# Performance work log

Hardware: AMD Instinct MI355X
Metric: run time of the kernel (lower is better)

Reference implementation:

```python
import jax, jax.numpy as jnp
import numpy as np

# Mistral-7B layer-0 config
D, DKV, DFF, NH, NKV, HD, BLK, VOCAB = 4096, 1024, 14336, 32, 8, 128, 64, 32000
THETA = 10000.0
NF4_CODE = jnp.array([-1.0, -0.6961928009986877, -0.5250730514526367, -0.39491748809814453,
                      -0.28444138169288635, -0.18477343022823334, -0.09105003625154495, 0.0,
                      0.07958029955625534, 0.16093020141124725, 0.24611230194568634,
                      0.33791524171829224, 0.44070982933044434, 0.5626170039176941,
                      0.7229568362236023, 1.0], dtype=jnp.float32)


def dequant_nf4(idx, absmax):
    # idx: int [out,in] 4-bit codes; absmax: [numel/BLK] blockwise scales
    w = jnp.take(NF4_CODE, idx.reshape(-1, BLK)) * absmax[:, None]
    return w.reshape(idx.shape)


def rmsnorm(x, w, eps=1e-5):
    return x * jax.lax.rsqrt(jnp.mean(x * x, axis=-1, keepdims=True) + eps) * w


def rope(x, pos):
    # x: [B,S,H,HD] -- HF rotate-half convention
    half = HD // 2
    inv = 1.0 / (THETA ** (jnp.arange(0, half, dtype=jnp.float32) / half))
    f = pos[:, None] * inv[None, :]                      # [S, half]
    cos = jnp.concatenate([jnp.cos(f), jnp.cos(f)], -1)[None, :, None, :]
    sin = jnp.concatenate([jnp.sin(f), jnp.sin(f)], -1)[None, :, None, :]
    x1, x2 = x[..., :half], x[..., half:]
    rot = jnp.concatenate([-x2, x1], -1)
    return x * cos + rot * sin


def setup_inputs() -> dict:
    key = jax.random.key(0)
    ks = jax.random.split(key, 20)
    B, S = 4, 512
    inp = {}
    inp["input_ids"] = jax.random.randint(ks[0], (B, S), 0, VOCAB, dtype=jnp.int32)
    inp["attention_mask"] = jnp.ones((B, S), dtype=jnp.int32)
    inp["embed_table"] = jax.random.normal(ks[1], (VOCAB, D), dtype=jnp.float32) * 0.02
    shapes = {"q": (D, D), "k": (DKV, D), "v": (DKV, D), "o": (D, D),
              "gate": (DFF, D), "up": (DFF, D), "down": (D, DFF)}
    for i, (n, sh) in enumerate(shapes.items()):
        inp["idx_" + n] = jax.random.randint(ks[2 + i], sh, 0, 16, dtype=jnp.int32)
        inp["absmax_" + n] = jax.random.uniform(ks[9 + i], (sh[0] * sh[1] // BLK,), dtype=jnp.float32) * 0.02
    inp["rms1_w"] = jnp.ones((D,), jnp.float32)
    inp["rms2_w"] = jnp.ones((D,), jnp.float32)
    inp["dp_w"] = jax.random.normal(ks[16], (50, D), jnp.float32) * 0.02
    inp["dp_b"] = jnp.zeros((50,), jnp.float32)
    return inp


def reference(input_ids, attention_mask, embed_table,
              idx_q, idx_k, idx_v, idx_o, idx_gate, idx_up, idx_down,
              absmax_q, absmax_k, absmax_v, absmax_o, absmax_gate, absmax_up, absmax_down,
              rms1_w, rms2_w, dp_w, dp_b):
    B, S = input_ids.shape
    h = embed_table[input_ids]                            # [B,S,D]

    # --- Mistral decoder layer 0 (hidden_states[1]) ---
    r = rmsnorm(h, rms1_w)
    Wq = dequant_nf4(idx_q, absmax_q)
    Wk = dequant_nf4(idx_k, absmax_k)
    Wv = dequant_nf4(idx_v, absmax_v)
    Wo = dequant_nf4(idx_o, absmax_o)
    q = (r @ Wq.T).reshape(B, S, NH, HD)
    k = (r @ Wk.T).reshape(B, S, NKV, HD)
    v = (r @ Wv.T).reshape(B, S, NKV, HD)
    pos = jnp.arange(S, dtype=jnp.float32)
    q, k = rope(q, pos), rope(k, pos)
    rep = NH // NKV
    k = jnp.repeat(k, rep, axis=2)
    v = jnp.repeat(v, rep, axis=2)
    scores = jnp.einsum('bqhd,bkhd->bhqk', q, k) / np.float32(np.sqrt(HD))
    causal = jnp.tril(jnp.ones((S, S), bool))
    m = causal[None, None] & (attention_mask[:, None, None, :] > 0)
    scores = jnp.where(m, scores, jnp.float32(-1e9))
    p = jax.nn.softmax(scores, axis=-1)
    ao = jnp.einsum('bhqk,bkhd->bqhd', p, v).reshape(B, S, D)
    h = h + ao @ Wo.T

    r2 = rmsnorm(h, rms2_w)
    Wg = dequant_nf4(idx_gate, absmax_gate)
    Wu = dequant_nf4(idx_up, absmax_up)
    Wd = dequant_nf4(idx_down, absmax_down)
    h = h + (jax.nn.silu(r2 @ Wg.T) * (r2 @ Wu.T)) @ Wd.T

    # --- last_token_pool + L2 normalize ---
    last = jnp.sum(attention_mask, axis=-1) - 1           # [B]
    pooled = h[jnp.arange(B), last]                       # [B,D]
    pooled = pooled / jnp.maximum(jnp.linalg.norm(pooled, axis=1, keepdims=True), 1e-12)

    # --- down_projection + query*entity node embeddings ---
    emb = pooled @ dp_w.T + dp_b                          # [B,50]
    bs = B // 2
    node = emb[:bs] * emb[bs:]                            # [bs,50]
    return node
```

## Files before the change

### kernel.cpp

```cpp
#include <hip/hip_runtime.h>
#include <stdint.h>
#include <math.h>

#define TOK 2048
#define DMODEL 4096
#define DFF 14336
#define SEQ 512

typedef float f32x4 __attribute__((ext_vector_type(4)));
typedef float f32x2 __attribute__((ext_vector_type(2)));
typedef short s16x8 __attribute__((ext_vector_type(8)));
typedef unsigned short u16x8 __attribute__((ext_vector_type(8)));

__constant__ float NF4_TAB[16] = {
  -1.0f, -0.6961928009986877f, -0.5250730514526367f, -0.39491748809814453f,
  -0.28444138169288635f, -0.18477343022823334f, -0.09105003625154495f, 0.0f,
  0.07958029955625534f, 0.16093020141124725f, 0.24611230194568634f,
  0.33791524171829224f, 0.44070982933044434f, 0.5626170039176941f,
  0.7229568362236023f, 1.0f };

__device__ __forceinline__ uint16_t f2bf(float f) {
  union { float f; uint32_t u; } x; x.f = f;
  uint32_t r = (x.u + 0x7FFFu + ((x.u >> 16) & 1u)) >> 16;
  return (uint16_t)r;
}
__device__ __forceinline__ float bf2f(uint16_t u) {
  union { uint32_t u; float f; } x; x.u = ((uint32_t)u) << 16;
  return x.f;
}
__device__ __forceinline__ f32x4 mfma16(s16x8 a, s16x8 b, f32x4 c) {
  return __builtin_amdgcn_mfma_f32_16x16x32_bf16(a, b, c, 0, 0, 0);
}
__device__ __forceinline__ void gload_lds16(const void* g, void* l) {
  __builtin_amdgcn_global_load_lds(
    (const __attribute__((address_space(1))) unsigned int*)g,
    (__attribute__((address_space(3))) unsigned int*)l, 16, 0, 0);
}
__device__ __forceinline__ f32x2 pf(float w, f32x2 v, f32x2 acc) {
  f32x2 wv = {w, w};
  return wv * v + acc;
}

__global__ __launch_bounds__(256) void k_fusedA(const int* __restrict__ ids,
    const float* __restrict__ table, const float* __restrict__ w1,
    uint16_t* __restrict__ rbuf, const int* __restrict__ idxK,
    const float* __restrict__ amK, const int* __restrict__ idxV,
    const float* __restrict__ amV, uint16_t* __restrict__ wbuf,
    const int* __restrict__ maskp, int* __restrict__ lastb)
{
  int bid = blockIdx.x, tid = threadIdx.x;
  if (bid < 2048) {
    int t = bid;
    int wv = tid >> 6, l = tid & 63;
    const float* src = table + (size_t)ids[t] * DMODEL;
    int d0 = tid * 16;
    float vals[16];
    float ss = 0.f;
    #pragma unroll
    for (int i = 0; i < 4; ++i) {
      float4 v4 = *(const float4*)(src + d0 + i * 4);
      vals[i*4+0] = v4.x; vals[i*4+1] = v4.y; vals[i*4+2] = v4.z; vals[i*4+3] = v4.w;
      ss += v4.x*v4.x + v4.y*v4.y + v4.z*v4.z + v4.w*v4.w;
    }
    #pragma unroll
    for (int off = 1; off < 64; off <<= 1) ss += __shfl_xor(ss, off);
    __shared__ float red[4];
    if (l == 0) red[wv] = ss;
    __syncthreads();
    float rs = rsqrtf((red[0]+red[1]+red[2]+red[3]) * (1.f/DMODEL) + 1e-5f);
    #pragma unroll
    for (int cth = 0; cth < 2; ++cth) {
      int dd = d0 + cth * 8;
      u16x8 pk;
      #pragma unroll
      for (int j = 0; j < 8; ++j) pk[j] = f2bf(vals[cth*8+j] * rs * w1[dd + j]);
      int dsw = (dd & ~63) | (((((dd >> 3) & 7) ^ (t & 7))) << 3);
      *(u16x8*)(rbuf + (size_t)t * DMODEL + dsw) = pk;
    }
  } else if (bid < 3072) {
    bool isV = bid >= 2560;
    const int* idx = isV ? idxV : idxK;
    const float* am = isV ? amV : amK;
    uint16_t* out = wbuf + (isV ? (size_t)1024 * DMODEL : 0);
    int base = bid - (isV ? 2560 : 2048);
    __shared__ float code[16];
    if (tid < 16) code[tid] = NF4_TAB[tid];
    __syncthreads();
    const int nch = 1024 * DMODEL / 8;
    for (int c = base * 256 + tid; c < nch; c += 512 * 256) {
      int e = c << 3;
      int row = e >> 12;
      int kc = e & 4095;
      float a = am[c >> 3];
      int4 i0 = *(const int4*)(idx + e);
      int4 i1 = *(const int4*)(idx + e + 4);
      u16x8 pk;
      pk[0] = f2bf(code[i0.x] * a);
      pk[1] = f2bf(code[i0.y] * a);
      pk[2] = f2bf(code[i0.z] * a);
      pk[3] = f2bf(code[i0.w] * a);
      pk[4] = f2bf(code[i1.x] * a);
      pk[5] = f2bf(code[i1.y] * a);
      pk[6] = f2bf(code[i1.z] * a);
      pk[7] = f2bf(code[i1.w] * a);
      int dk = (kc & ~63) | (((((kc >> 3) & 7) ^ (row & 7))) << 3);
      *(u16x8*)(out + (size_t)row * DMODEL + dk) = pk;
    }
  } else {
    int b = bid - 3072;
    if (tid < 64) {
      int cnt = 0;
      for (int j = tid; j < SEQ; j += 64) cnt += (maskp[b * SEQ + j] > 0);
      #pragma unroll
      for (int off = 1; off < 64; off <<= 1) cnt += __shfl_xor(cnt, off);
      if (tid == 0) lastb[b] = cnt - 1;
    }
  }
}

__global__ __launch_bounds__(512, 2) void k_gemmkv(
    const uint16_t* __restrict__ A, const uint16_t* __restrict__ W,
    float* __restrict__ pout)
{
  constexpr int K = 4096;
  constexpr int NT = 16;
  __shared__ __align__(1024) uint16_t As_[2 * 256 * 64];
  __shared__ __align__(1024) uint16_t Bs_[2 * 256 * 64];
  const int tid = threadIdx.x;
  const int wid = tid >> 6, l = tid & 63;
  const int wr = wid >> 2, wc = wid & 3;
  int f = blockIdx.x + (blockIdx.y << 3) + (blockIdx.z << 6);
  int fs = ((f & 7) << 5) + (f >> 3);
  const int n0 = (fs & 7) * 256;
  const int m0 = ((fs >> 3) & 7) * 256;
  const int zq = fs >> 6;
  const size_t kbase = (size_t)zq * 1024;
  const int lrow = l >> 3, lcb = (l & 7) * 16;

  auto stA = [&](int t, int h) {
    int ta = (t < NT) ? t : (t - NT);
    const char* g = (const char*)A +
        ((size_t)(m0 + h * 128 + wid * 16 + lrow) * K + kbase + ta * 64) * 2 + lcb;
    char* s = (char*)As_ + (t & 1) * 32768 + h * 16384 + wid * 2048;
    gload_lds16(g, s);
    gload_lds16(g + (size_t)8 * K * 2, s + 1024);
  };
  auto stB = [&](int t, int h) {
    int ta = (t < NT) ? t : (t - NT);
    const char* g = (const char*)W +
        ((size_t)(n0 + h * 128 + wid * 16 + lrow) * K + kbase + ta * 64) * 2 + lcb;
    char* s = (char*)Bs_ + (t & 1) * 32768 + h * 16384 + wid * 2048;
    gload_lds16(g, s);
    gload_lds16(g + (size_t)8 * K * 2, s + 1024);
  };

  const int cb0 = (((l >> 4) << 4)) ^ ((l & 7) << 4);
  const int cb1 = (64 + ((l >> 4) << 4)) ^ ((l & 7) << 4);

  const f32x4 Z4 = {0.f, 0.f, 0.f, 0.f};
// ... 36 lines not shown
  }

  stB(0, 0); stA(0, 0); stB(0, 1); stA(0, 1);
  stB(1, 0); stA(1, 0); stB(1, 1);
  VMW;
  __builtin_amdgcn_s_barrier();

  for (int it = 0; it < NT / 2; ++it) {
    int t0 = 2 * it, t1 = t0 + 1;
    PHASE(0, 0, 1, stA(t1, 1));
    PHASE(0, 1, 0, stB(t0 + 2, 0));
    PHASE(0, 2, 0, stA(t0 + 2, 0));
    PHASE(0, 3, 0, { stB(t0 + 2, 1); VMW; });
    PHASE(1, 0, 1, stA(t0 + 2, 1));
    PHASE(1, 1, 0, stB(t1 + 2, 0));
    PHASE(1, 2, 0, stA(t1 + 2, 0));
    PHASE(1, 3, 0, { stB(t1 + 2, 1); VMW; });
  }
  asm volatile("s_waitcnt vmcnt(0)" ::: "memory");
  __builtin_amdgcn_s_barrier();
#undef PHASE
#undef VMW

  float* po = pout + (size_t)zq * 2048 * 2048;
  #pragma unroll
  for (int mf = 0; mf < 8; ++mf)
    #pragma unroll
    for (int nf = 0; nf < 4; ++nf)
      #pragma unroll
      for (int r = 0; r < 4; ++r) {
        int row = m0 + (2 * mf + wr) * 16 + ((l >> 4) << 2) + r;
        int col = n0 + wc * 64 + nf * 16 + (l & 15);
        po[(size_t)row * 2048 + col] = acc[mf][nf][r];
      }
}

__global__ __launch_bounds__(256) void k_prep_r4(const uint16_t* __restrict__ rbuf,
    const int* __restrict__ lastb, float* __restrict__ r4i)
{
  int r = blockIdx.x;
  int t = r * SEQ + lastb[r];
  const uint16_t* src = rbuf + (size_t)t * DMODEL;
  for (int k = threadIdx.x * 8; k < DMODEL; k += 2048) {
    int so = (k & ~63) | (((((k >> 3) & 7) ^ (t & 7))) << 3);
    u16x8 v = *(const u16x8*)(src + so);
    #pragma unroll
    for (int j = 0; j < 8; ++j) r4i[(k + j) * 4 + r] = bf2f(v[j]);
  }
}

__global__ __launch_bounds__(256) void k_fusedD(const float* __restrict__ p,
    uint16_t* __restrict__ kv, const int* __restrict__ idxQ,
    const float* __restrict__ amQ, const float* __restrict__ a4i,
    float* __restrict__ q4i)
{
  int bid = blockIdx.x, tid = threadIdx.x;
  if (bid < 2048) {
    int t = bid;
    const size_t zs = (size_t)2048 * 2048;
    auto sum4 = [&](int c) -> float {
      size_t o = (size_t)t * 2048 + c;
      return p[o] + p[o + zs] + p[o + 2 * zs] + p[o + 3 * zs];
    };
    float pos = (float)(t & (SEQ - 1));
    for (int pi = tid; pi < 512; pi += 256) {
      int hh = pi >> 6, j = pi & 63;
      int c1 = hh * 128 + j, c2 = c1 + 64;
      float s1 = sum4(c1), s2 = sum4(c2);
      float f = pos * expf(-(float)j * 0.14391156831212787f);
      float sn, cs;
      sincosf(f, &sn, &cs);
      kv[(size_t)t * 2048 + c1] = f2bf(s1 * cs - s2 * sn);
      kv[(size_t)t * 2048 + c2] = f2bf(s2 * cs + s1 * sn);
    }
    for (int c = 1024 + tid; c < 2048; c += 256)
      kv[(size_t)t * 2048 + c] = f2bf(sum4(c));
  } else {
    __shared__ float code[16];
    if (tid < 16) code[tid] = NF4_TAB[tid];
    __syncthreads();
    int wv = tid >> 6, l = tid & 63;
    int lhi = l >> 4;
    int n = (bid - 2048) * 4 + wv;
    const int4* ip = (const int4*)(idxQ + (size_t)n * 4096);
    const float* ap = amQ + (size_t)n * 64;
    f32x2 a01 = {0.f, 0.f}, a23 = {0.f, 0.f};
    #pragma unroll
    for (int kk = 0; kk < 16; ++kk) {
      int4 iv = ip[kk * 64 + l];
      float sc = ap[kk * 4 + lhi];
      float w0 = code[iv.x] * sc, w1 = code[iv.y] * sc;
      float w2 = code[iv.z] * sc, w3 = code[iv.w] * sc;
      const float* A0 = a4i + (kk * 256 + l * 4) * 4;
      f32x4 k0 = *(const f32x4*)(A0);
      f32x4 k1 = *(const f32x4*)(A0 + 4);
      f32x4 k2 = *(const f32x4*)(A0 + 8);
      f32x4 k3 = *(const f32x4*)(A0 + 12);
      a01 = pf(w0, __builtin_shufflevector(k0, k0, 0, 1), a01);
      a23 = pf(w0, __builtin_shufflevector(k0, k0, 2, 3), a23);
      a01 = pf(w1, __builtin_shufflevector(k1, k1, 0, 1), a01);
      a23 = pf(w1, __builtin_shufflevector(k1, k1, 2, 3), a23);
      a01 = pf(w2, __builtin_shufflevector(k2, k2, 0, 1), a01);
      a23 = pf(w2, __builtin_shufflevector(k2, k2, 2, 3), a23);
      a01 = pf(w3, __builtin_shufflevector(k3, k3, 0, 1), a01);
      a23 = pf(w3, __builtin_shufflevector(k3, k3, 2, 3), a23);
    }
    float a0 = a01[0], a1 = a01[1], a2 = a23[0], a3 = a23[1];
    #pragma unroll
    for (int off = 1; off < 64; off <<= 1) {
      a0 += __shfl_xor(a0, off); a1 += __shfl_xor(a1, off);
      a2 += __shfl_xor(a2, off); a3 += __shfl_xor(a3, off);
    }
    if (l == 0) {
      f32x4 o;
      o[0] = a0; o[1] = a1; o[2] = a2; o[3] = a3;
      *(f32x4*)(q4i + (size_t)n * 4) = o;
    }
  }
}

__global__ __launch_bounds__(256) void k_gemv_o(const int* __restrict__ idx,
    const float* __restrict__ am, const float* __restrict__ a4i,
    float* __restrict__ out4i, const float* __restrict__ table,
    const int* __restrict__ ids, const int* __restrict__ lastb)
{
  __shared__ float code[16];
  if (threadIdx.x < 16) code[threadIdx.x] = NF4_TAB[threadIdx.x];
  __syncthreads();
  int wv = threadIdx.x >> 6, l = threadIdx.x & 63;
  int lhi = l >> 4;
  int n = blockIdx.x * 4 + wv;
  const int4* ip = (const int4*)(idx + (size_t)n * 4096);
  const float* ap = am + (size_t)n * 64;
  f32x2 a01 = {0.f, 0.f}, a23 = {0.f, 0.f};
  #pragma unroll
  for (int kk = 0; kk < 16; ++kk) {
    int4 iv = ip[kk * 64 + l];
    float sc = ap[kk * 4 + lhi];
    float w0 = code[iv.x] * sc, w1 = code[iv.y] * sc;
    float w2 = code[iv.z] * sc, w3 = code[iv.w] * sc;
// ... 9 lines not shown
    a01 = pf(w2, __builtin_shufflevector(k2, k2, 0, 1), a01);
    a23 = pf(w2, __builtin_shufflevector(k2, k2, 2, 3), a23);
    a01 = pf(w3, __builtin_shufflevector(k3, k3, 0, 1), a01);
    a23 = pf(w3, __builtin_shufflevector(k3, k3, 2, 3), a23);
  }
  float a0 = a01[0], a1 = a01[1], a2 = a23[0], a3 = a23[1];
  #pragma unroll
  for (int off = 1; off < 64; off <<= 1) {
    a0 += __shfl_xor(a0, off); a1 += __shfl_xor(a1, off);
    a2 += __shfl_xor(a2, off); a3 += __shfl_xor(a3, off);
  }
  if (l == 0) {
    f32x4 o;
    o[0] = a0; o[1] = a1; o[2] = a2; o[3] = a3;
    #pragma unroll
    for (int r = 0; r < 4; ++r)
      o[r] += table[(size_t)ids[r * SEQ + lastb[r]] * DMODEL + n];
    *(f32x4*)(out4i + (size_t)n * 4) = o;
  }
}

__global__ __launch_bounds__(256) void k_gemv_gu(const int* __restrict__ idxg,
    const float* __restrict__ amg, const int* __restrict__ idxu,
    const float* __restrict__ amu, const float* __restrict__ a4i,
    float* __restrict__ hm4i)
{
  __shared__ float code[16];
  if (threadIdx.x < 16) code[threadIdx.x] = NF4_TAB[threadIdx.x];
  __syncthreads();
  int wv = threadIdx.x >> 6, l = threadIdx.x & 63;
  int lhi = l >> 4;
  int n = blockIdx.x * 4 + wv;
  const int4* ipg = (const int4*)(idxg + (size_t)n * 4096);
  const int4* ipu = (const int4*)(idxu + (size_t)n * 4096);
  const float* apg = amg + (size_t)n * 64;
  const float* apu = amu + (size_t)n * 64;
  f32x2 g01 = {0.f, 0.f}, g23 = {0.f, 0.f};
  f32x2 u01 = {0.f, 0.f}, u23 = {0.f, 0.f};
  #pragma unroll 8
  for (int kk = 0; kk < 16; ++kk) {
    int4 ig = ipg[kk * 64 + l];
    int4 iu = ipu[kk * 64 + l];
    float sg = apg[kk * 4 + lhi];
    float su = apu[kk * 4 + lhi];
    float wg0 = code[ig.x] * sg, wg1 = code[ig.y] * sg;
    float wg2 = code[ig.z] * sg, wg3 = code[ig.w] * sg;
    float wu0 = code[iu.x] * su, wu1 = code[iu.y] * su;
    float wu2 = code[iu.z] * su, wu3 = code[iu.w] * su;
    const float* A0 = a4i + (kk * 256 + l * 4) * 4;
    f32x4 k0 = *(const f32x4*)(A0);
    f32x4 k1 = *(const f32x4*)(A0 + 4);
    f32x4 k2 = *(const f32x4*)(A0 + 8);
    f32x4 k3 = *(const f32x4*)(A0 + 12);
    f32x2 k0l = __builtin_shufflevector(k0, k0, 0, 1), k0h = __builtin_shufflevector(k0, k0, 2, 3);
    f32x2 k1l = __builtin_shufflevector(k1, k1, 0, 1), k1h = __builtin_shufflevector(k1, k1, 2, 3);
    f32x2 k2l = __builtin_shufflevector(k2, k2, 0, 1), k2h = __builtin_shufflevector(k2, k2, 2, 3);
    f32x2 k3l = __builtin_shufflevector(k3, k3, 0, 1), k3h = __builtin_shufflevector(k3, k3, 2, 3);
    g01 = pf(wg0, k0l, g01); g23 = pf(wg0, k0h, g23);
    g01 = pf(wg1, k1l, g01); g23 = pf(wg1, k1h, g23);
    g01 = pf(wg2, k2l, g01); g23 = pf(wg2, k2h, g23);
    g01 = pf(wg3, k3l, g01); g23 = pf(wg3, k3h, g23);
    u01 = pf(wu0, k0l, u01); u23 = pf(wu0, k0h, u23);
    u01 = pf(wu1, k1l, u01); u23 = pf(wu1, k1h, u23);
    u01 = pf(wu2, k2l, u01); u23 = pf(wu2, k2h, u23);
    u01 = pf(wu3, k3l, u01); u23 = pf(wu3, k3h, u23);
  }
  float g0 = g01[0], g1 = g01[1], g2 = g23[0], g3 = g23[1];
  float u0 = u01[0], u1 = u01[1], u2 = u23[0], u3 = u23[1];
  #pragma unroll
  for (int off = 1; off < 64; off <<= 1) {
    g0 += __shfl_xor(g0, off); g1 += __shfl_xor(g1, off);
    g2 += __shfl_xor(g2, off); g3 += __shfl_xor(g3, off);
    u0 += __shfl_xor(u0, off); u1 += __shfl_xor(u1, off);
    u2 += __shfl_xor(u2, off); u3 += __shfl_xor(u3, off);
  }
  if (l == 0) {
// ... 34 lines not shown
    a23 = pf(w0, __builtin_shufflevector(k0, k0, 2, 3), a23);
    a01 = pf(w1, __builtin_shufflevector(k1, k1, 0, 1), a01);
    a23 = pf(w1, __builtin_shufflevector(k1, k1, 2, 3), a23);
    a01 = pf(w2, __builtin_shufflevector(k2, k2, 0, 1), a01);
    a23 = pf(w2, __builtin_shufflevector(k2, k2, 2, 3), a23);
    a01 = pf(w3, __builtin_shufflevector(k3, k3, 0, 1), a01);
    a23 = pf(w3, __builtin_shufflevector(k3, k3, 2, 3), a23);
  }
  float a0 = a01[0], a1 = a01[1], a2 = a23[0], a3 = a23[1];
  #pragma unroll
  for (int off = 1; off < 64; off <<= 1) {
    a0 += __shfl_xor(a0, off); a1 += __shfl_xor(a1, off);
    a2 += __shfl_xor(a2, off); a3 += __shfl_xor(a3, off);
  }
  if (l == 0) {
    f32x4 hr = *(const f32x4*)(h4i + (size_t)n * 4);
    h4r[0 * 4096 + n] = hr[0] + a0;
    h4r[1 * 4096 + n] = hr[1] + a1;
    h4r[2 * 4096 + n] = hr[2] + a2;
    h4r[3 * 4096 + n] = hr[3] + a3;
  }
}

__global__ __launch_bounds__(256) void k_attn4(const float* __restrict__ q4i,
    const uint16_t* __restrict__ kv, const int* __restrict__ maskp,
    const int* __restrict__ lastb, float* __restrict__ ao4i)
{
  int hh = blockIdx.x, b = blockIdx.y;
  int kvh = hh >> 2;
  int tid = threadIdx.x;
  __shared__ float qs[128];
  __shared__ float sarr[512];
  __shared__ float red[256];
  __shared__ f32x2 oacc2[4][64];
  int last = lastb[b];
  if (tid < 128) {
    int d = tid, j = d & 63;
    float f = (float)last * expf(-(float)j * 0.14391156831212787f);
    float sn, cs;
    sincosf(f, &sn, &cs);
    float qd  = q4i[(hh * 128 + d) * 4 + b];
    float qd2 = (d < 64) ? q4i[(hh * 128 + d + 64) * 4 + b]
                         : q4i[(hh * 128 + d - 64) * 4 + b];
    float v = (d < 64) ? (qd * cs - qd2 * sn) : (qd * cs + qd2 * sn);
    qs[d] = v * 0.08838834764831845f;
  }
  __syncthreads();
  float sl[2];
  #pragma unroll
  for (int h2 = 0; h2 < 2; ++h2) {
    int jj = tid + h2 * 256;
    bool valid = (jj <= last) && (maskp[b * SEQ + jj] > 0);
    float s = -1e9f;
    if (valid) {
      s = 0.f;
      const uint16_t* kp = kv + ((size_t)(b * SEQ + jj)) * 2048 + kvh * 128;
      #pragma unroll
      for (int c = 0; c < 16; ++c) {
        u16x8 kvv = *(const u16x8*)(kp + c * 8);
        #pragma unroll
        for (int e = 0; e < 8; ++e)
          s = fmaf(qs[c * 8 + e], bf2f(kvv[e]), s);
      }
    }
    sarr[jj] = s;
    sl[h2] = s;
  }
  red[tid] = fmaxf(sl[0], sl[1]);
  __syncthreads();
  for (int s = 128; s > 0; s >>= 1) {
    if (tid < s) red[tid] = fmaxf(red[tid], red[tid + s]);
    __syncthreads();
  }
  float m = red[0];
  __syncthreads();
  float ps = 0.f;
  #pragma unroll
  for (int h2 = 0; h2 < 2; ++h2) {
    int jj = tid + h2 * 256;
    float pe = __expf(sarr[jj] - m);
    ps += pe;
    sarr[jj] = pe;
  }
  red[tid] = ps;
  __syncthreads();
  for (int s = 128; s > 0; s >>= 1) {
    if (tid < s) red[tid] += red[tid + s];
    __syncthreads();
  }
  float inv = 1.f / red[0];
  __syncthreads();
  int qd = tid >> 6, pr = tid & 63;
  f32x2 acc = {0.f, 0.f};
  const uint16_t* vp = kv + ((size_t)(b * SEQ + qd * 128)) * 2048 + 1024 + kvh * 128 + pr * 2;
  for (int j = 0; j < 128; ++j) {
    float pj = sarr[qd * 128 + j];
    uint32_t pair = *(const uint32_t*)(vp + (size_t)j * 2048);
    f32x2 v;
    v[0] = bf2f((uint16_t)(pair & 0xffff));
    v[1] = bf2f((uint16_t)(pair >> 16));
    acc = pf(pj, v, acc);
  }
  oacc2[qd][pr] = acc;
  __syncthreads();
  if (tid < 64) {
    f32x2 s = oacc2[0][tid] + oacc2[1][tid] + oacc2[2][tid] + oacc2[3][tid];
    ao4i[((size_t)(hh * 128 + tid * 2)) * 4 + b]     = s[0] * inv;
    ao4i[((size_t)(hh * 128 + tid * 2 + 1)) * 4 + b] = s[1] * inv;
  }
}

__global__ __launch_bounds__(256) void k_rms2i(const float* __restrict__ h4i,
    const float* __restrict__ w, float* __restrict__ r2i)
{
  int tid = threadIdx.x, wv = tid >> 6, l = tid & 63;
  f32x4 vals[16];
  f32x4 ss = {0.f, 0.f, 0.f, 0.f};
  #pragma unroll
  for (int i = 0; i < 16; ++i) {
    vals[i] = *(const f32x4*)(h4i + (size_t)(tid + i * 256) * 4);
    ss += vals[i] * vals[i];
  }
  #pragma unroll
  for (int off = 1; off < 64; off <<= 1) {
    ss[0] += __shfl_xor(ss[0], off);
    ss[1] += __shfl_xor(ss[1], off);
    ss[2] += __shfl_xor(ss[2], off);
    ss[3] += __shfl_xor(ss[3], off);
  }
  __shared__ f32x4 red[4];
  if (l == 0) red[wv] = ss;
  __syncthreads();
  f32x4 tot = red[0] + red[1] + red[2] + red[3];
  f32x4 rs;
  #pragma unroll
  for (int r = 0; r < 4; ++r) rs[r] = rsqrtf(tot[r] * (1.f / 4096.f) + 1e-5f);
  #pragma unroll
  for (int i = 0; i < 16; ++i) {
    float wk = w[tid + i * 256];
    f32x4 o = vals[i] * rs * wk;
    *(f32x4*)(r2i + (size_t)(tid + i * 256) * 4) = o;
  }
}

__global__ __launch_bounds__(256) void k_pool3(const float* __restrict__ h4r,
    const float* __restrict__ dpw, const float* __restrict__ dpb,
    float* __restrict__ out)
{
  int o = blockIdx.x;
  int tid = threadIdx.x, wv = tid >> 6, l = tid & 63;
  __shared__ float dsh[4], nsh[4];
  const float* row = h4r + wv * 4096;
  const float* wrow = dpw + (size_t)o * 4096;
  float d1 = 0.f, ss = 0.f;
  for (int d = l * 4; d < 4096; d += 256) {
    float4 v = *(const float4*)(row + d);
    float4 u = *(const float4*)(wrow + d);
    d1 += v.x*u.x + v.y*u.y + v.z*u.z + v.w*u.w;
    ss += v.x*v.x + v.y*v.y + v.z*v.z + v.w*v.w;
  }
  #pragma unroll
  for (int off = 1; off < 64; off <<= 1) {
    d1 += __shfl_xor(d1, off);
    ss += __shfl_xor(ss, off);
  }
  if (l == 0) { dsh[wv] = d1; nsh[wv] = fmaxf(sqrtf(ss), 1e-12f); }
  __syncthreads();
// ... 11 lines not shown
  const int*   ids   = (const int*)d_in[0];
  const int*   maskp = (const int*)d_in[1];
  const float* table = (const float*)d_in[2];
  const int* idxp[7];
  const float* amp[7];
  if (in_sizes[4] == in_sizes[3] / 64) {
    for (int i = 0; i < 7; ++i) {
      idxp[i] = (const int*)d_in[3 + 2 * i];
      amp[i]  = (const float*)d_in[4 + 2 * i];
    }
  } else {
    for (int i = 0; i < 7; ++i) {
      idxp[i] = (const int*)d_in[3 + i];
      amp[i]  = (const float*)d_in[10 + i];
    }
  }
  const float* rms1 = (const float*)d_in[17];
  const float* rms2w = (const float*)d_in[18];
  const float* dpw  = (const float*)d_in[19];
  const float* dpb  = (const float*)d_in[20];
  float* out = (float*)d_out;

  char* p = (char*)d_ws;
  int*      lastb = (int*)p;      p += 256;
  float*    r4i   = (float*)p;    p += 4 * 4096 * 4;
  float*    q4i   = (float*)p;    p += 4 * 4096 * 4;
  float*    ao4i  = (float*)p;    p += 4 * 4096 * 4;
  float*    h4i   = (float*)p;    p += 4 * 4096 * 4;
  float*    r2i   = (float*)p;    p += 4 * 4096 * 4;
  float*    h4r   = (float*)p;    p += 4 * 4096 * 4;
  float*    hm4i  = (float*)p;    p += (size_t)4 * DFF * 4 + 512;
  uint16_t* kvbuf = (uint16_t*)p; p += (size_t)TOK * 2048 * 2;
  uint16_t* rbuf  = (uint16_t*)p; p += (size_t)TOK * DMODEL * 2;
  uint16_t* wbuf  = (uint16_t*)p; p += (size_t)2048 * DMODEL * 2;
  float*    pbuf  = (float*)p;    p += (size_t)4 * 2048 * 2048 * 4;

  k_fusedA<<<3076, 256, 0, stream>>>(ids, table, rms1, rbuf,
      idxp[1], amp[1], idxp[2], amp[2], wbuf, maskp, lastb);

  k_gemmkv<<<dim3(8, 8, 4), 512, 0, stream>>>(rbuf, wbuf, pbuf);

  k_prep_r4<<<4, 256, 0, stream>>>(rbuf, lastb, r4i);

  k_fusedD<<<3072, 256, 0, stream>>>(pbuf, kvbuf, idxp[0], amp[0], r4i, q4i);

  k_attn4<<<dim3(32, 4), 256, 0, stream>>>(q4i, kvbuf, maskp, lastb, ao4i);

  k_gemv_o<<<1024, 256, 0, stream>>>(idxp[3], amp[3], ao4i, h4i, table, ids, lastb);

  k_rms2i<<<1, 256, 0, stream>>>(h4i, rms2w, r2i);
  k_gemv_gu<<<3584, 256, 0, stream>>>(idxp[4], amp[4], idxp[5], amp[5], r2i, hm4i);
  k_gemv_down<<<1024, 256, 0, stream>>>(idxp[6], amp[6], hm4i, h4i, h4r);

  k_pool3<<<50, 256, 0, stream>>>(h4r, dpw, dpb, out);
}
```

Baseline: 390.3 us.

## Skip V projection over all tokens by applying Wv after attention-weighted averaging

Only the last token's output is needed, so V is no longer projected for every token. The attention probabilities instead average the normalized inputs per KV head (rbar), and Wv is applied once to that small result through a GEMV. The batched GEMM now computes only K, which halves its size. Scores are computed per token directly from the summed K partials with RoPE, and the second RMSNorm is folded into the gate/up GEMV. This removes a large share of GEMM work and the V write, at the cost of several new kernels and a serial per-token loop in the rbar step.

```diff
diff --git a/kernel.cpp b/kernel.cpp
--- a/kernel.cpp
+++ b/kernel.cpp
@@ -44,9 +44,9 @@
 __global__ __launch_bounds__(256) void k_fusedA(const int* __restrict__ ids,
     const float* __restrict__ table, const float* __restrict__ w1,
     uint16_t* __restrict__ rbuf, const int* __restrict__ idxK,
-    const float* __restrict__ amK, const int* __restrict__ idxV,
-    const float* __restrict__ amV, uint16_t* __restrict__ wbuf,
-    const int* __restrict__ maskp, int* __restrict__ lastb)
+    const float* __restrict__ amK, uint16_t* __restrict__ wbuf,
+    const int* __restrict__ maskp, int* __restrict__ lastb,
+    float* __restrict__ r4i)
 {
   int bid = blockIdx.x, tid = threadIdx.x;
   if (bid < 2048) {
@@ -77,12 +77,8 @@
       int dsw = (dd & ~63) | (((((dd >> 3) & 7) ^ (t & 7))) << 3);
       *(u16x8*)(rbuf + (size_t)t * DMODEL + dsw) = pk;
     }
-  } else if (bid < 3072) {
-    bool isV = bid >= 2560;
-    const int* idx = isV ? idxV : idxK;
-    const float* am = isV ? amV : amK;
-    uint16_t* out = wbuf + (isV ? (size_t)1024 * DMODEL : 0);
-    int base = bid - (isV ? 2560 : 2048);
+  } else if (bid < 2560) {
+    int base = bid - 2048;
     __shared__ float code[16];
     if (tid < 16) code[tid] = NF4_TAB[tid];
     __syncthreads();
@@ -91,9 +87,9 @@
       int e = c << 3;
       int row = e >> 12;
       int kc = e & 4095;
-      float a = am[c >> 3];
-      int4 i0 = *(const int4*)(idx + e);
-      int4 i1 = *(const int4*)(idx + e + 4);
+      float a = amK[c >> 3];
+      int4 i0 = *(const int4*)(idxK + e);
+      int4 i1 = *(const int4*)(idxK + e + 4);
       u16x8 pk;
       pk[0] = f2bf(code[i0.x] * a);
       pk[1] = f2bf(code[i0.y] * a);
@@ -104,37 +100,107 @@
       pk[6] = f2bf(code[i1.z] * a);
       pk[7] = f2bf(code[i1.w] * a);
       int dk = (kc & ~63) | (((((kc >> 3) & 7) ^ (row & 7))) << 3);
-      *(u16x8*)(out + (size_t)row * DMODEL + dk) = pk;
+      *(u16x8*)(wbuf + (size_t)row * DMODEL + dk) = pk;
     }
   } else {
-    int b = bid - 3072;
-    if (tid < 64) {
-      int cnt = 0;
-      for (int j = tid; j < SEQ; j += 64) cnt += (maskp[b * SEQ + j] > 0);
-      #pragma unroll
-      for (int off = 1; off < 64; off <<= 1) cnt += __shfl_xor(cnt, off);
-      if (tid == 0) lastb[b] = cnt - 1;
+    int b = bid - 2560;
+    int wv = tid >> 6, l = tid & 63;
+    __shared__ int redi[4];
+    __shared__ float redf[4];
+    int cnt = 0;
+    for (int j = tid; j < SEQ; j += 256) cnt += (maskp[b * SEQ + j] > 0);
+    #pragma unroll
+    for (int off = 1; off < 64; off <<= 1) cnt += __shfl_xor(cnt, off);
+    if (l == 0) redi[wv] = cnt;
+    __syncthreads();
+    int last = redi[0] + redi[1] + redi[2] + redi[3] - 1;
+    if (tid == 0) lastb[b] = last;
+    int t = b * SEQ + last;
+    const float* src = table + (size_t)ids[t] * DMODEL;
+    int d0 = tid * 16;
+    float vals[16];
+    float ss = 0.f;
+    #pragma unroll
+    for (int i = 0; i < 4; ++i) {
+      float4 v4 = *(const float4*)(src + d0 + i * 4);
+      vals[i*4+0] = v4.x; vals[i*4+1] = v4.y; vals[i*4+2] = v4.z; vals[i*4+3] = v4.w;
+      ss += v4.x*v4.x + v4.y*v4.y + v4.z*v4.z + v4.w*v4.w;
     }
-  }
-}
-
-__global__ __launch_bounds__(512, 2) void k_gemmkv(
+    #pragma unroll
+    for (int off = 1; off < 64; off <<= 1) ss += __shfl_xor(ss, off);
+    if (l == 0) redf[wv] = ss;
+    __syncthreads();
+    float rs = rsqrtf((redf[0]+redf[1]+redf[2]+redf[3]) * (1.f/DMODEL) + 1e-5f);
+    #pragma unroll
+    for (int i = 0; i < 16; ++i)
+      r4i[(d0 + i) * 4 + b] = vals[i] * rs * w1[d0 + i];
+  }
+}
+
+__global__ __launch_bounds__(256) void k_gemv_q(const int* __restrict__ idx,
+    const float* __restrict__ am, const float* __restrict__ a4i,
+    float* __restrict__ q4p)
+{
+  __shared__ float code[16];
+  if (threadIdx.x < 16) code[threadIdx.x] = NF4_TAB[threadIdx.x];
+  __syncthreads();
+  int wv = threadIdx.x >> 6, l = threadIdx.x & 63;
+  int lhi = l >> 4;
+  int n = blockIdx.x * 4 + wv;
+  const int4* ip = (const int4*)(idx + (size_t)n * 4096);
+  const float* ap = am + (size_t)n * 64;
+  f32x2 a01 = {0.f, 0.f}, a23 = {0.f, 0.f};
+  #pragma unroll
+  for (int kk = 0; kk < 16; ++kk) {
+    int4 iv = ip[kk * 64 + l];
+    float sc = ap[kk * 4 + lhi];
+    float w0 = code[iv.x] * sc, w1 = code[iv.y] * sc;
+    float w2 = code[iv.z] * sc, w3 = code[iv.w] * sc;
+    const float* A0 = a4i + (kk * 256 + l * 4) * 4;
+    f32x4 k0 = *(const f32x4*)(A0);
+    f32x4 k1 = *(const f32x4*)(A0 + 4);
+    f32x4 k2 = *(const f32x4*)(A0 + 8);
+    f32x4 k3 = *(const f32x4*)(A0 + 12);
+    a01 = pf(w0, __builtin_shufflevector(k0, k0, 0, 1), a01);
+    a23 = pf(w0, __builtin_shufflevector(k0, k0, 2, 3), a23);
+    a01 = pf(w1, __builtin_shufflevector(k1, k1, 0, 1), a01);
+    a23 = pf(w1, __builtin_shufflevector(k1, k1, 2, 3), a23);
+    a01 = pf(w2, __builtin_shufflevector(k2, k2, 0, 1), a01);
+    a23 = pf(w2, __builtin_shufflevector(k2, k2, 2, 3), a23);
+    a01 = pf(w3, __builtin_shufflevector(k3, k3, 0, 1), a01);
+    a23 = pf(w3, __builtin_shufflevector(k3, k3, 2, 3), a23);
+  }
+  float a0 = a01[0], a1 = a01[1], a2 = a23[0], a3 = a23[1];
+  #pragma unroll
+  for (int off = 1; off < 64; off <<= 1) {
+    a0 += __shfl_xor(a0, off); a1 += __shfl_xor(a1, off);
+    a2 += __shfl_xor(a2, off); a3 += __shfl_xor(a3, off);
+  }
+  if (l == 0) {
+    q4p[0 * 4096 + n] = a0;
+    q4p[1 * 4096 + n] = a1;
+    q4p[2 * 4096 + n] = a2;
+    q4p[3 * 4096 + n] = a3;
+  }
+}
+
+__global__ __launch_bounds__(512, 2) void k_gemmk(
     const uint16_t* __restrict__ A, const uint16_t* __restrict__ W,
     float* __restrict__ pout)
 {
   constexpr int K = 4096;
-  constexpr int NT = 16;
+  constexpr int NT = 8;
   __shared__ __align__(1024) uint16_t As_[2 * 256 * 64];
   __shared__ __align__(1024) uint16_t Bs_[2 * 256 * 64];
   const int tid = threadIdx.x;
   const int wid = tid >> 6, l = tid & 63;
   const int wr = wid >> 2, wc = wid & 3;
-  int f = blockIdx.x + (blockIdx.y << 3) + (blockIdx.z << 6);
-  int fs = ((f & 7) << 5) + (f >> 3);
-  const int n0 = (fs & 7) * 256;
-  const int m0 = ((fs >> 3) & 7) * 256;
-  const int zq = fs >> 6;
-  const size_t kbase = (size_t)zq * 1024;
+  int f = blockIdx.x + (blockIdx.y << 2) + (blockIdx.z << 5);
+  int fs = ((f & 7) << 5) | (f >> 3);
+  const int n0 = (fs & 3) * 256;
+  const int m0 = ((fs >> 2) & 7) * 256;
+  const int zq = fs >> 5;
+  const size_t kbase = (size_t)zq * 512;
   const int lrow = l >> 3, lcb = (l & 7) * 16;
 
   auto stA = [&](int t, int h) {
@@ -217,7 +283,7 @@
 #undef PHASE
 #undef VMW
 
-  float* po = pout + (size_t)zq * 2048 * 2048;
+  float* po = pout + (size_t)zq * 2048 * 1024;
   #pragma unroll
   for (int mf = 0; mf < 8; ++mf)
     #pragma unroll
@@ -226,91 +292,197 @@
       for (int r = 0; r < 4; ++r) {
         int row = m0 + (2 * mf + wr) * 16 + ((l >> 4) << 2) + r;
         int col = n0 + wc * 64 + nf * 16 + (l & 15);
-        po[(size_t)row * 2048 + col] = acc[mf][nf][r];
+        po[(size_t)row * 1024 + col] = acc[mf][nf][r];
       }
 }
 
-__global__ __launch_bounds__(256) void k_prep_r4(const uint16_t* __restrict__ rbuf,
-    const int* __restrict__ lastb, float* __restrict__ r4i)
-{
-  int r = blockIdx.x;
-  int t = r * SEQ + lastb[r];
-  const uint16_t* src = rbuf + (size_t)t * DMODEL;
-  for (int k = threadIdx.x * 8; k < DMODEL; k += 2048) {
-    int so = (k & ~63) | (((((k >> 3) & 7) ^ (t & 7))) << 3);
-    u16x8 v = *(const u16x8*)(src + so);
-    #pragma unroll
-    for (int j = 0; j < 8; ++j) r4i[(k + j) * 4 + r] = bf2f(v[j]);
-  }
-}
-
-__global__ __launch_bounds__(256) void k_fusedD(const float* __restrict__ p,
-    uint16_t* __restrict__ kv, const int* __restrict__ idxQ,
-    const float* __restrict__ amQ, const float* __restrict__ a4i,
-    float* __restrict__ q4i)
-{
-  int bid = blockIdx.x, tid = threadIdx.x;
-  if (bid < 2048) {
-    int t = bid;
-    const size_t zs = (size_t)2048 * 2048;
-    auto sum4 = [&](int c) -> float {
-      size_t o = (size_t)t * 2048 + c;
-      return p[o] + p[o + zs] + p[o + 2 * zs] + p[o + 3 * zs];
-    };
-    float pos = (float)(t & (SEQ - 1));
-    for (int pi = tid; pi < 512; pi += 256) {
-      int hh = pi >> 6, j = pi & 63;
-      int c1 = hh * 128 + j, c2 = c1 + 64;
-      float s1 = sum4(c1), s2 = sum4(c2);
-      float f = pos * expf(-(float)j * 0.14391156831212787f);
-      float sn, cs;
-      sincosf(f, &sn, &cs);
-      kv[(size_t)t * 2048 + c1] = f2bf(s1 * cs - s2 * sn);
-      kv[(size_t)t * 2048 + c2] = f2bf(s2 * cs + s1 * sn);
+__global__ __launch_bounds__(256) void k_kscore(const float* __restrict__ pbuf,
+    const float* __restrict__ q4p, const int* __restrict__ lastb,
+    float* __restrict__ scores)
+{
+  int t = blockIdx.x;
+  int b = t >> 9, s = t & 511;
+  int tid = threadIdx.x;
+  __shared__ float qrot[4096];
+  __shared__ float ksum[1024];
+  __shared__ float cq[64], sq[64], ck[64], sk[64];
+  int last = lastb[b];
+  if (tid < 64) {
+    float inv = expf(-(float)tid * 0.14391156831212787f);
+    float s1, c1, s2, c2;
+    sincosf((float)last * inv, &s1, &c1);
+    sincosf((float)s * inv, &s2, &c2);
+    cq[tid] = c1; sq[tid] = s1; ck[tid] = c2; sk[tid] = s2;
+  }
+  __syncthreads();
+  const float scale = 0.08838834764831845f;
+  #pragma unroll
+  for (int i = 0; i < 16; ++i) {
+    int flat = tid + i * 256;
+    int d = flat & 127, j = d & 63;
+    float qa  = q4p[b * 4096 + flat];
+    float qb2 = q4p[b * 4096 + (flat ^ 64)];
+    float v = (d < 64) ? qa * cq[j] - qb2 * sq[j] : qa * cq[j] + qb2 * sq[j];
+    qrot[flat] = v * scale;
+  }
+  int c0 = tid * 4;
+  f32x4 ks = {0.f, 0.f, 0.f, 0.f};
+  #pragma unroll
+  for (int z = 0; z < 8; ++z)
+    ks += *(const f32x4*)(pbuf + (size_t)z * 2048 * 1024 + (size_t)t * 1024 + c0);
+  *(f32x4*)(ksum + c0) = ks;
+  __syncthreads();
+  f32x4 part = *(const f32x4*)(ksum + (c0 ^ 64));
+  f32x4 krv;
+  #pragma unroll
+  for (int e = 0; e < 4; ++e) {
+    int c = c0 + e, j = c & 63;
+    krv[e] = ((c & 64) == 0) ? ks[e] * ck[j] - part[e] * sk[j]
+                             : ks[e] * ck[j] + part[e] * sk[j];
+  }
+  int kvh = tid >> 5;
+  float p0 = 0.f, p1 = 0.f, p2 = 0.f, p3 = 0.f;
+  #pragma unroll
+  for (int e = 0; e < 4; ++e) {
+    int d = (c0 + e) & 127;
+    float kv = krv[e];
+    p0 = fmaf(qrot[(kvh * 4 + 0) * 128 + d], kv, p0);
+    p1 = fmaf(qrot[(kvh * 4 + 1) * 128 + d], kv, p1);
+    p2 = fmaf(qrot[(kvh * 4 + 2) * 128 + d], kv, p2);
+    p3 = fmaf(qrot[(kvh * 4 + 3) * 128 + d], kv, p3);
+  }
+  #pragma unroll
+  for (int off = 1; off < 32; off <<= 1) {
+    p0 += __shfl_xor(p0, off); p1 += __shfl_xor(p1, off);
+    p2 += __shfl_xor(p2, off); p3 += __shfl_xor(p3, off);
+  }
+  if ((tid & 31) == 0) {
+    scores[((b * 32 + kvh * 4 + 0) << 9) + s] = p0;
+    scores[((b * 32 + kvh * 4 + 1) << 9) + s] = p1;
+    scores[((b * 32 + kvh * 4 + 2) << 9) + s] = p2;
+    scores[((b * 32 + kvh * 4 + 3) << 9) + s] = p3;
+  }
+}
+
+__global__ __launch_bounds__(256) void k_smrbar(const float* __restrict__ scores,
+    const uint16_t* __restrict__ rbuf, const int* __restrict__ maskp,
+    const int* __restrict__ lastb, float* __restrict__ rbar)
+{
+  int bx = blockIdx.x;
+  int hg = bx & 3, ds = (bx >> 2) & 3, b = (bx >> 4) & 3, jq = bx >> 6;
+  int tid = threadIdx.x, wv = tid >> 6, l = tid & 63;
+  __shared__ float p[8][512];
+  __shared__ float red[4];
+  int last = lastb[b];
+  for (int i = 0; i < 8; ++i) {
+    int hh = hg * 8 + i;
+    int j0 = tid, j1 = tid + 256;
+    bool ok0 = (j0 <= last) && (maskp[b * 512 + j0] > 0);
+    bool ok1 = (j1 <= last) && (maskp[b * 512 + j1] > 0);
+    float s0 = ok0 ? scores[((b * 32 + hh) << 9) + j0] : -1e9f;
+    float s1v = ok1 ? scores[((b * 32 + hh) << 9) + j1] : -1e9f;
+    float m = fmaxf(s0, s1v);
+    #pragma unroll
+    for (int off = 1; off < 64; off <<= 1) m = fmaxf(m, __shfl_xor(m, off));
+    if (l == 0) red[wv] = m;
+    __syncthreads();
+    m = fmaxf(fmaxf(red[0], red[1]), fmaxf(red[2], red[3]));
+    __syncthreads();
+    float e0 = __expf(s0 - m), e1 = __expf(s1v - m);
+    float sum = e0 + e1;
+    #pragma unroll
+    for (int off = 1; off < 64; off <<= 1) sum += __shfl_xor(sum, off);
+    if (l == 0) red[wv] = sum;
+    __syncthreads();
+    float inv = 1.f / (red[0] + red[1] + red[2] + red[3]);
+    __syncthreads();
+    p[i][j0] = e0 * inv;
+    p[i][j1] = e1 * inv;
+  }
+  __syncthreads();
+  int d = ds * 1024 + tid * 4;
+  int gb = d & ~63, chnk = (d >> 3) & 7, rem = d & 7;
+  float acc[8][4];
+  #pragma unroll
+  for (int i = 0; i < 8; ++i)
+    #pragma unroll
+    for (int e = 0; e < 4; ++e) acc[i][e] = 0.f;
+  int jbase = jq * 256;
+  int jend = (last < jbase + 255) ? last : (jbase + 255);
+  for (int j = jbase; j <= jend; ++j) {
+    int t = b * 512 + j;
+    const uint16_t* row = rbuf + (size_t)t * 4096;
+    int so = gb + ((chnk ^ (t & 7)) << 3) + rem;
+    ushort4 rv = *(const ushort4*)(row + so);
+    float r0 = bf2f(rv.x), r1 = bf2f(rv.y), r2 = bf2f(rv.z), r3 = bf2f(rv.w);
+    #pragma unroll
+    for (int i = 0; i < 8; ++i) {
+      float pj = p[i][j];
+      acc[i][0] = fmaf(pj, r0, acc[i][0]);
+      acc[i][1] = fmaf(pj, r1, acc[i][1]);
+      acc[i][2] = fmaf(pj, r2, acc[i][2]);
+      acc[i][3] = fmaf(pj, r3, acc[i][3]);
     }
-    for (int c = 1024 + tid; c < 2048; c += 256)
-      kv[(size_t)t * 2048 + c] = f2bf(sum4(c));
-  } else {
-    __shared__ float code[16];
-    if (tid < 16) code[tid] = NF4_TAB[tid];
-    __syncthreads();
-    int wv = tid >> 6, l = tid & 63;
-    int lhi = l >> 4;
-    int n = (bid - 2048) * 4 + wv;
-    const int4* ip = (const int4*)(idxQ + (size_t)n * 4096);
-    const float* ap = amQ + (size_t)n * 64;
-    f32x2 a01 = {0.f, 0.f}, a23 = {0.f, 0.f};
-    #pragma unroll
-    for (int kk = 0; kk < 16; ++kk) {
-      int4 iv = ip[kk * 64 + l];
-      float sc = ap[kk * 4 + lhi];
-      float w0 = code[iv.x] * sc, w1 = code[iv.y] * sc;
-      float w2 = code[iv.z] * sc, w3 = code[iv.w] * sc;
-      const float* A0 = a4i + (kk * 256 + l * 4) * 4;
-      f32x4 k0 = *(const f32x4*)(A0);
-      f32x4 k1 = *(const f32x4*)(A0 + 4);
-      f32x4 k2 = *(const f32x4*)(A0 + 8);
-      f32x4 k3 = *(const f32x4*)(A0 + 12);
-      a01 = pf(w0, __builtin_shufflevector(k0, k0, 0, 1), a01);
-      a23 = pf(w0, __builtin_shufflevector(k0, k0, 2, 3), a23);
-      a01 = pf(w1, __builtin_shufflevector(k1, k1, 0, 1), a01);
-      a23 = pf(w1, __builtin_shufflevector(k1, k1, 2, 3), a23);
-      a01 = pf(w2, __builtin_shufflevector(k2, k2, 0, 1), a01);
-      a23 = pf(w2, __builtin_shufflevector(k2, k2, 2, 3), a23);
-      a01 = pf(w3, __builtin_shufflevector(k3, k3, 0, 1), a01);
-      a23 = pf(w3, __builtin_shufflevector(k3, k3, 2, 3), a23);
+  }
+  #pragma unroll
+  for (int i = 0; i < 8; ++i) {
+    int hh = hg * 8 + i;
+    int kvh = hh >> 2, g = hh & 3;
+    #pragma unroll
+    for (int e = 0; e < 4; ++e)
+      rbar[(((size_t)jq * 8 + kvh) * 4096 + d + e) * 16 + g * 4 + b] = acc[i][e];
+  }
+}
+
+__global__ __launch_bounds__(256) void k_gemv_v(const int* __restrict__ idx,
+    const float* __restrict__ am, const float* __restrict__ rbar,
+    float* __restrict__ ao4i)
+{
+  __shared__ float code[16];
+  if (threadIdx.x < 16) code[threadIdx.x] = NF4_TAB[threadIdx.x];
+  __syncthreads();
+  int wv = threadIdx.x >> 6, l = threadIdx.x & 63;
+  int lhi = l >> 4;
+  int n = blockIdx.x * 4 + wv;
+  int kvh = n >> 7, dout = n & 127;
+  const int4* ip = (const int4*)(idx + (size_t)n * 4096);
+  const float* ap = am + (size_t)n * 64;
+  const float* rb0 = rbar + (size_t)kvh * 4096 * 16;
+  const float* rb1 = rb0 + (size_t)8 * 4096 * 16;
+  f32x4 acc[4];
+  #pragma unroll
+  for (int g = 0; g < 4; ++g) acc[g] = (f32x4){0.f, 0.f, 0.f, 0.f};
+  #pragma unroll 4
+  for (int kk = 0; kk < 16; ++kk) {
+    int4 iv = ip[kk * 64 + l];
+    float sc = ap[kk * 4 + lhi];
+    float w[4];
+    w[0] = code[iv.x] * sc; w[1] = code[iv.y] * sc;
+    w[2] = code[iv.z] * sc; w[3] = code[iv.w] * sc;
+    int k0 = kk * 256 + l * 4;
+    #pragma unroll
+    for (int e = 0; e < 4; ++e) {
+      const float* base0 = rb0 + (size_t)(k0 + e) * 16;
+      const float* base1 = rb1 + (size_t)(k0 + e) * 16;
+      f32x4 we = {w[e], w[e], w[e], w[e]};
+      #pragma unroll
+      for (int g = 0; g < 4; ++g) {
+        f32x4 v = *(const f32x4*)(base0 + g * 4) + *(const f32x4*)(base1 + g * 4);
+        acc[g] += we * v;
+      }
     }
-    float a0 = a01[0], a1 = a01[1], a2 = a23[0], a3 = a23[1];
-    #pragma unroll
-    for (int off = 1; off < 64; off <<= 1) {
-      a0 += __shfl_xor(a0, off); a1 += __shfl_xor(a1, off);
-      a2 += __shfl_xor(a2, off); a3 += __shfl_xor(a3, off);
-    }
-    if (l == 0) {
-      f32x4 o;
-      o[0] = a0; o[1] = a1; o[2] = a2; o[3] = a3;
-      *(f32x4*)(q4i + (size_t)n * 4) = o;
-    }
+  }
+  #pragma unroll
+  for (int g = 0; g < 4; ++g)
+    #pragma unroll
+    for (int c = 0; c < 4; ++c)
+      #pragma unroll
+      for (int off = 1; off < 64; off <<= 1)
+        acc[g][c] += __shfl_xor(acc[g][c], off);
+  if (l == 0) {
+    #pragma unroll
+    for (int g = 0; g < 4; ++g)
+      *(f32x4*)(ao4i + (size_t)((kvh * 4 + g) * 128 + dout) * 4) = acc[g];
   }
 }
 
@@ -366,13 +538,32 @@
 
 __global__ __launch_bounds__(256) void k_gemv_gu(const int* __restrict__ idxg,
     const float* __restrict__ amg, const int* __restrict__ idxu,
-    const float* __restrict__ amu, const float* __restrict__ a4i,
-    float* __restrict__ hm4i)
+    const float* __restrict__ amu, const float* __restrict__ h4i,
+    const float* __restrict__ w2, float* __restrict__ hm4i)
 {
   __shared__ float code[16];
-  if (threadIdx.x < 16) code[threadIdx.x] = NF4_TAB[threadIdx.x];
-  __syncthreads();
-  int wv = threadIdx.x >> 6, l = threadIdx.x & 63;
+  __shared__ f32x4 redv[4];
+  int tid = threadIdx.x, wv = tid >> 6, l = tid & 63;
+  if (tid < 16) code[tid] = NF4_TAB[tid];
+  f32x4 ssv = {0.f, 0.f, 0.f, 0.f};
+  for (int i = 0; i < 16; ++i) {
+    f32x4 h = *(const f32x4*)(h4i + (size_t)(tid + i * 256) * 4);
+    ssv += h * h;
+  }
+  #pragma unroll
+  for (int off = 1; off < 64; off <<= 1) {
+    ssv[0] += __shfl_xor(ssv[0], off);
+    ssv[1] += __shfl_xor(ssv[1], off);
+    ssv[2] += __shfl_xor(ssv[2], off);
+    ssv[3] += __shfl_xor(ssv[3], off);
+  }
+  if (l == 0) redv[wv] = ssv;
+  __syncthreads();
+  f32x4 tot = redv[0] + redv[1] + redv[2] + redv[3];
+  f32x4 rs;
+  #pragma unroll
+  for (int r = 0; r < 4; ++r) rs[r] = rsqrtf(tot[r] * (1.f / 4096.f) + 1e-5f);
+
   int lhi = l >> 4;
   int n = blockIdx.x * 4 + wv;
   const int4* ipg = (const int4*)(idxg + (size_t)n * 4096);
@@ -391,11 +582,13 @@
     float wg2 = code[ig.z] * sg, wg3 = code[ig.w] * sg;
     float wu0 = code[iu.x] * su, wu1 = code[iu.y] * su;
     float wu2 = code[iu.z] * su, wu3 = code[iu.w] * su;
-    const float* A0 = a4i + (kk * 256 + l * 4) * 4;
-    f32x4 k0 = *(const f32x4*)(A0);
-    f32x4 k1 = *(const f32x4*)(A0 + 4);
-    f32x4 k2 = *(const f32x4*)(A0 + 8);
-    f32x4 k3 = *(const f32x4*)(A0 + 12);
+    int kb = kk * 256 + l * 4;
+    const float* H = h4i + (size_t)kb * 4;
+    float4 w2v = *(const float4*)(w2 + kb);
+    f32x4 k0 = (*(const f32x4*)(H))      * rs * w2v.x;
+    f32x4 k1 = (*(const f32x4*)(H + 4))  * rs * w2v.y;
+    f32x4 k2 = (*(const f32x4*)(H + 8))  * rs * w2v.z;
+    f32x4 k3 = (*(const f32x4*)(H + 12)) * rs * w2v.w;
     f32x2 k0l = __builtin_shufflevector(k0, k0, 0, 1), k0h = __builtin_shufflevector(k0, k0, 2, 3);
     f32x2 k1l = __builtin_shufflevector(k1, k1, 0, 1), k1h = __builtin_shufflevector(k1, k1, 2, 3);
     f32x2 k2l = __builtin_shufflevector(k2, k2, 0, 1), k2h = __builtin_shufflevector(k2, k2, 2, 3);
@@ -476,127 +669,6 @@
   }
 }
 
-__global__ __launch_bounds__(256) void k_attn4(const float* __restrict__ q4i,
-    const uint16_t* __restrict__ kv, const int* __restrict__ maskp,
-    const int* __restrict__ lastb, float* __restrict__ ao4i)
-{
-  int hh = blockIdx.x, b = blockIdx.y;
-  int kvh = hh >> 2;
-  int tid = threadIdx.x;
-  __shared__ float qs[128];
-  __shared__ float sarr[512];
-  __shared__ float red[256];
-  __shared__ f32x2 oacc2[4][64];
-  int last = lastb[b];
-  if (tid < 128) {
-    int d = tid, j = d & 63;
-    float f = (float)last * expf(-(float)j * 0.14391156831212787f);
-    float sn, cs;
-    sincosf(f, &sn, &cs);
-    float qd  = q4i[(hh * 128 + d) * 4 + b];
-    float qd2 = (d < 64) ? q4i[(hh * 128 + d + 64) * 4 + b]
-                         : q4i[(hh * 128 + d - 64) * 4 + b];
-    float v = (d < 64) ? (qd * cs - qd2 * sn) : (qd * cs + qd2 * sn);
-    qs[d] = v * 0.08838834764831845f;
-  }
-  __syncthreads();
-  float sl[2];
-  #pragma unroll
-  for (int h2 = 0; h2 < 2; ++h2) {
-    int jj = tid + h2 * 256;
-    bool valid = (jj <= last) && (maskp[b * SEQ + jj] > 0);
-    float s = -1e9f;
-    if (valid) {
-      s = 0.f;
-      const uint16_t* kp = kv + ((size_t)(b * SEQ + jj)) * 2048 + kvh * 128;
-      #pragma unroll
-      for (int c = 0; c < 16; ++c) {
-        u16x8 kvv = *(const u16x8*)(kp + c * 8);
-        #pragma unroll
-        for (int e = 0; e < 8; ++e)
-          s = fmaf(qs[c * 8 + e], bf2f(kvv[e]), s);
-      }
-    }
-    sarr[jj] = s;
-    sl[h2] = s;
-  }
-  red[tid] = fmaxf(sl[0], sl[1]);
-  __syncthreads();
-  for (int s = 128; s > 0; s >>= 1) {
-    if (tid < s) red[tid] = fmaxf(red[tid], red[tid + s]);
-    __syncthreads();
-  }
-  float m = red[0];
-  __syncthreads();
-  float ps = 0.f;
-  #pragma unroll
-  for (int h2 = 0; h2 < 2; ++h2) {
-    int jj = tid + h2 * 256;
-    float pe = __expf(sarr[jj] - m);
-    ps += pe;
-    sarr[jj] = pe;
-  }
-  red[tid] = ps;
-  __syncthreads();
-  for (int s = 128; s > 0; s >>= 1) {
-    if (tid < s) red[tid] += red[tid + s];
-    __syncthreads();
-  }
-  float inv = 1.f / red[0];
-  __syncthreads();
-  int qd = tid >> 6, pr = tid & 63;
-  f32x2 acc = {0.f, 0.f};
-  const uint16_t* vp = kv + ((size_t)(b * SEQ + qd * 128)) * 2048 + 1024 + kvh * 128 + pr * 2;
-  for (int j = 0; j < 128; ++j) {
-    float pj = sarr[qd * 128 + j];
-    uint32_t pair = *(const uint32_t*)(vp + (size_t)j * 2048);
-    f32x2 v;
-    v[0] = bf2f((uint16_t)(pair & 0xffff));
-    v[1] = bf2f((uint16_t)(pair >> 16));
-    acc = pf(pj, v, acc);
-  }
-  oacc2[qd][pr] = acc;
-  __syncthreads();
-  if (tid < 64) {
-    f32x2 s = oacc2[0][tid] + oacc2[1][tid] + oacc2[2][tid] + oacc2[3][tid];
-    ao4i[((size_t)(hh * 128 + tid * 2)) * 4 + b]     = s[0] * inv;
-    ao4i[((size_t)(hh * 128 + tid * 2 + 1)) * 4 + b] = s[1] * inv;
-  }
-}
-
-__global__ __launch_bounds__(256) void k_rms2i(const float* __restrict__ h4i,
-    const float* __restrict__ w, float* __restrict__ r2i)
-{
-  int tid = threadIdx.x, wv = tid >> 6, l = tid & 63;
-  f32x4 vals[16];
-  f32x4 ss = {0.f, 0.f, 0.f, 0.f};
-  #pragma unroll
-  for (int i = 0; i < 16; ++i) {
-    vals[i] = *(const f32x4*)(h4i + (size_t)(tid + i * 256) * 4);
-    ss += vals[i] * vals[i];
-  }
-  #pragma unroll
-  for (int off = 1; off < 64; off <<= 1) {
-    ss[0] += __shfl_xor(ss[0], off);
-    ss[1] += __shfl_xor(ss[1], off);
-    ss[2] += __shfl_xor(ss[2], off);
-    ss[3] += __shfl_xor(ss[3], off);
-  }
-  __shared__ f32x4 red[4];
-  if (l == 0) red[wv] = ss;
-  __syncthreads();
-  f32x4 tot = red[0] + red[1] + red[2] + red[3];
-  f32x4 rs;
-  #pragma unroll
-  for (int r = 0; r < 4; ++r) rs[r] = rsqrtf(tot[r] * (1.f / 4096.f) + 1e-5f);
-  #pragma unroll
-  for (int i = 0; i < 16; ++i) {
-    float wk = w[tid + i * 256];
-    f32x4 o = vals[i] * rs * wk;
-    *(f32x4*)(r2i + (size_t)(tid + i * 256) * 4) = o;
-  }
-}
-
 __global__ __launch_bounds__(256) void k_pool3(const float* __restrict__ h4r,
     const float* __restrict__ dpw, const float* __restrict__ dpb,
     float* __restrict__ out)
@@ -654,34 +726,35 @@
   float* out = (float*)d_out;
 
   char* p = (char*)d_ws;
-  int*      lastb = (int*)p;      p += 256;
-  float*    r4i   = (float*)p;    p += 4 * 4096 * 4;
-  float*    q4i   = (float*)p;    p += 4 * 4096 * 4;
-  float*    ao4i  = (float*)p;    p += 4 * 4096 * 4;
-  float*    h4i   = (float*)p;    p += 4 * 4096 * 4;
-  float*    r2i   = (float*)p;    p += 4 * 4096 * 4;
-  float*    h4r   = (float*)p;    p += 4 * 4096 * 4;
-  float*    hm4i  = (float*)p;    p += (size_t)4 * DFF * 4 + 512;
-  uint16_t* kvbuf = (uint16_t*)p; p += (size_t)TOK * 2048 * 2;
-  uint16_t* rbuf  = (uint16_t*)p; p += (size_t)TOK * DMODEL * 2;
-  uint16_t* wbuf  = (uint16_t*)p; p += (size_t)2048 * DMODEL * 2;
-  float*    pbuf  = (float*)p;    p += (size_t)4 * 2048 * 2048 * 4;
-
-  k_fusedA<<<3076, 256, 0, stream>>>(ids, table, rms1, rbuf,
-      idxp[1], amp[1], idxp[2], amp[2], wbuf, maskp, lastb);
-
-  k_gemmkv<<<dim3(8, 8, 4), 512, 0, stream>>>(rbuf, wbuf, pbuf);
-
-  k_prep_r4<<<4, 256, 0, stream>>>(rbuf, lastb, r4i);
-
-  k_fusedD<<<3072, 256, 0, stream>>>(pbuf, kvbuf, idxp[0], amp[0], r4i, q4i);
-
-  k_attn4<<<dim3(32, 4), 256, 0, stream>>>(q4i, kvbuf, maskp, lastb, ao4i);
+  int*      lastb  = (int*)p;      p += 256;
+  float*    r4i    = (float*)p;    p += 4 * 4096 * 4;
+  float*    q4p    = (float*)p;    p += 4 * 4096 * 4;
+  float*    ao4i   = (float*)p;    p += 4 * 4096 * 4;
+  float*    h4i    = (float*)p;    p += 4 * 4096 * 4;
+  float*    h4r    = (float*)p;    p += 4 * 4096 * 4;
+  float*    scores = (float*)p;    p += 4 * 32 * 512 * 4;
+  float*    hm4i   = (float*)p;    p += (size_t)4 * DFF * 4 + 512;
+  float*    rbar   = (float*)p;    p += (size_t)2 * 8 * 4096 * 16 * 4;
+  uint16_t* rbuf   = (uint16_t*)p; p += (size_t)TOK * DMODEL * 2;
+  uint16_t* wbuf   = (uint16_t*)p; p += (size_t)1024 * DMODEL * 2;
+  float*    pbuf   = (float*)p;    p += (size_t)8 * 2048 * 1024 * 4;
+
+  k_fusedA<<<2564, 256, 0, stream>>>(ids, table, rms1, rbuf,
+      idxp[1], amp[1], wbuf, maskp, lastb, r4i);
+
+  k_gemv_q<<<1024, 256, 0, stream>>>(idxp[0], amp[0], r4i, q4p);
+
+  k_gemmk<<<dim3(4, 8, 8), 512, 0, stream>>>(rbuf, wbuf, pbuf);
+
+  k_kscore<<<2048, 256, 0, stream>>>(pbuf, q4p, lastb, scores);
+
+  k_smrbar<<<128, 256, 0, stream>>>(scores, rbuf, maskp, lastb, rbar);
+
+  k_gemv_v<<<256, 256, 0, stream>>>(idxp[2], amp[2], rbar, ao4i);
 
   k_gemv_o<<<1024, 256, 0, stream>>>(idxp[3], amp[3], ao4i, h4i, table, ids, lastb);
 
-  k_rms2i<<<1, 256, 0, stream>>>(h4i, rms2w, r2i);
-  k_gemv_gu<<<3584, 256, 0, stream>>>(idxp[4], amp[4], idxp[5], amp[5], r2i, hm4i);
+  k_gemv_gu<<<3584, 256, 0, stream>>>(idxp[4], amp[4], idxp[5], amp[5], h4i, rms2w, hm4i);
   k_gemv_down<<<1024, 256, 0, stream>>>(idxp[6], amp[6], hm4i, h4i, h4r);
 
   k_pool3<<<50, 256, 0, stream>>>(h4r, dpw, dpb, out);
```

After: 540.4 us. +38.5%, slower.
